# Performance work log

Measured on AMD Instinct MI355X. Metric: run time of the kernel, lower is better.

Reference implementation:

```python
import math
import jax, jax.numpy as jnp
import numpy as np

B, S, D, H, V = 8, 1024, 512, 8, 32000
HD = D // H


def _position_embedding(seq_len, d_model):
    pos = jnp.arange(seq_len, dtype=jnp.float32)[:, None]                 # [S,1]
    div = jnp.exp(jnp.arange(0, d_model, 2, dtype=jnp.float32) * (-math.log(10000.0) / d_model))  # [D/2]
    ang = pos * div                                                        # [S,D/2]
    # interleave sin (even cols) / cos (odd cols)
    return jnp.stack([jnp.sin(ang), jnp.cos(ang)], axis=-1).reshape(seq_len, d_model)


def _min_max_normalize(w):
    lo = jnp.min(w, axis=-1, keepdims=True)
    hi = jnp.max(w, axis=-1, keepdims=True)
    return (w - lo) / (hi - lo)


def _converable_mask(h, Wc, bc):
    bs, seq = h.shape[0], h.shape[1]
    half = seq // 2
    shift = math.ceil(seq / 2)
    width = jnp.einsum('bsd,od->bso', h, Wc)[..., 0] + bc[0]               # [B,S]
    width = _min_max_normalize(width)[..., None]                           # [B,S,1]
    origin = jnp.concatenate([jnp.linspace(1.0, 0.0, half),
                              jnp.linspace(0.0, 1.0, seq - half)])         # [S]
    origin_mask = 1.0 - jax.nn.sigmoid((origin[None, None, :] - width) * 100.0)  # [B,S,S]
    idx = (jnp.arange(seq - 1, -1, -1)[:, None] + jnp.arange(seq)[None, :]) % seq  # [S,S]
    idx = jnp.roll(idx, shift, axis=0)
    # torch.roll of a [1,S] row along dim 0 is a no-op
    cmp = idx >= jnp.arange(seq)[None, :]                                  # [S,S] bool
    move = jnp.concatenate([cmp[:shift], ~cmp[shift:]], axis=0)            # [S,S]
    gathered = jnp.take_along_axis(origin_mask, idx[None, :, :], axis=2)   # [B,S,S]
    return gathered * move.astype(origin_mask.dtype)


def setup_inputs():
    key = jax.random.key(0)
    ks = jax.random.split(key, 9)
    s_emb = 1.0
    s_hd = 1.0 / math.sqrt(HD)
    s_d = 1.0 / math.sqrt(D)
    return {
        'x':   jax.random.randint(ks[0], (B, S), 0, V),
        'emb': jax.random.normal(ks[1], (V, D), dtype=jnp.float32) * s_emb,
        'Wq':  jax.random.normal(ks[2], (HD, HD), dtype=jnp.float32) * s_hd,
        'Wk':  jax.random.normal(ks[3], (HD, HD), dtype=jnp.float32) * s_hd,
        'Wv':  jax.random.normal(ks[4], (HD, HD), dtype=jnp.float32) * s_hd,
        'Wo':  jax.random.normal(ks[5], (D, D), dtype=jnp.float32) * s_d,
        'bo':  jnp.zeros((D,), dtype=jnp.float32),
        'Wc':  jax.random.normal(ks[6], (1, D), dtype=jnp.float32) * s_d,
        'bc':  jnp.zeros((1,), dtype=jnp.float32),
    }


def reference(x, emb, Wq, Wk, Wv, Wo, bo, Wc, bc):
    h = emb[x] + _position_embedding(S, D)[None]                           # [B,S,D]
    mask = _converable_mask(h, Wc, bc)                                     # [B,S,S]
    hh = h.reshape(B, S, H, HD)
    q = jnp.einsum('bshd,od->bsho', hh, Wq)
    k = jnp.einsum('bshd,od->bsho', hh, Wk)
    v = jnp.einsum('bshd,od->bsho', hh, Wv)
    energy = jnp.einsum('bqhd,bkhd->bhqk', q, k)                           # [B,H,S,S]
    # mask [B,S,S] broadcasts as [1,B,S,S]; valid because B == H (as in original)
    energy = energy * mask
    attn = jax.nn.softmax(energy / math.sqrt(D), axis=3)
    out = jnp.einsum('bhqk,bkhd->bqhd', attn, v).reshape(B, S, D)
    out = out @ Wo.T + bo
    return (out, mask)
```

## Files before the change

kernel.cpp:

```cpp
#include <hip/hip_runtime.h>
#include <hip/hip_bf16.h>
#include <math.h>

#define Bn 8
#define Sn 1024
#define Dn 512
#define Hn 8
#define HDn 64

typedef __bf16 bf16x8 __attribute__((ext_vector_type(8)));
typedef __bf16 bf16x4 __attribute__((ext_vector_type(4)));
typedef __bf16 bf16x2 __attribute__((ext_vector_type(2)));
typedef float  f32x4  __attribute__((ext_vector_type(4)));
typedef float  f32x16 __attribute__((ext_vector_type(16)));
typedef unsigned int u32x4 __attribute__((ext_vector_type(4)));
typedef int i32x2 __attribute__((ext_vector_type(2)));

__device__ __forceinline__ unsigned enc_f(float v) {
    unsigned u = __float_as_uint(v);
    return (u & 0x80000000u) ? ~u : (u | 0x80000000u);
}
__device__ __forceinline__ float dec_f(unsigned k) {
    unsigned u = (k & 0x80000000u) ? (k ^ 0x80000000u) : ~k;
    return __uint_as_float(u);
}

__global__ __launch_bounds__(256) void k_fused(
        const int* __restrict__ x, const float* __restrict__ emb,
        const float* __restrict__ Wc, const float* __restrict__ bc,
        const float* __restrict__ Wq, const float* __restrict__ Wk,
        const float* __restrict__ Wv,
        float* __restrict__ width, unsigned* __restrict__ lohi,
        __bf16* __restrict__ q, __bf16* __restrict__ k, __bf16* __restrict__ vt) {
    __shared__ __align__(16) __bf16 Xs[64][72];
    __shared__ __align__(16) __bf16 WqS[64][72];
    __shared__ __align__(16) __bf16 WkS[64][72];
    __shared__ __align__(16) __bf16 WvS[64][72];
    __shared__ float wtok[8];
    int t = threadIdx.x;
    int bs0 = blockIdx.x * 8;
    int m0 = blockIdx.x * 64;
    int w = t >> 6, lane = t & 63, quad = lane >> 4, li = lane & 15;

    {
        int token = t >> 5, l32 = t & 31;
        int bs = bs0 + token;
        int s = bs & (Sn - 1);
        int tok = x[bs];
        float wpart = 0.f;
        int row = token * 8 + ((l32 * 16) >> 6);
        #pragma unroll
        for (int j = 0; j < 4; ++j) {
            int d0 = l32 * 16 + j * 4;
            float4 ev = *(const float4*)&emb[(size_t)tok * Dn + d0];
            float4 wc = *(const float4*)&Wc[d0];
            float hv[4];
            #pragma unroll
            for (int i = 0; i < 4; ++i) {
                int d = d0 + i;
                float f = __expf((float)(d & ~1) * (-9.210340371976184f / 512.0f));
                float ang = (float)s * f;
                float pe = (d & 1) ? __cosf(ang) : __sinf(ang);
                hv[i] = (&ev.x)[i] + pe;
                wpart += hv[i] * (&wc.x)[i];
            }
            *(bf16x4*)&Xs[row][d0 & 63] =
                (bf16x4){(__bf16)hv[0], (__bf16)hv[1], (__bf16)hv[2], (__bf16)hv[3]};
        }
        #pragma unroll
        for (int off = 1; off < 32; off <<= 1) wpart += __shfl_xor(wpart, off);
        if (l32 == 0) { float wv = wpart + bc[0]; width[bs] = wv; wtok[token] = wv; }
    }
    #pragma unroll
    for (int it = 0; it < 4; ++it) {
        int e = (it * 256 + t) * 4; int r = e >> 6, c = e & 63;
        float4 qv = *(const float4*)&Wq[e];
        *(bf16x4*)&WqS[r][c] = (bf16x4){(__bf16)qv.x, (__bf16)qv.y, (__bf16)qv.z, (__bf16)qv.w};
        float4 kv = *(const float4*)&Wk[e];
        *(bf16x4*)&WkS[r][c] = (bf16x4){(__bf16)kv.x, (__bf16)kv.y, (__bf16)kv.z, (__bf16)kv.w};
        float4 vv = *(const float4*)&Wv[e];
        *(bf16x4*)&WvS[r][c] = (bf16x4){(__bf16)vv.x, (__bf16)vv.y, (__bf16)vv.z, (__bf16)vv.w};
    }
    __syncthreads();

    if (t == 0) {
        float mn = wtok[0], mx = wtok[0];
        #pragma unroll
        for (int i = 1; i < 8; ++i) { mn = fminf(mn, wtok[i]); mx = fmaxf(mx, wtok[i]); }
        int b = bs0 >> 10;
        atomicMin(&lohi[b], enc_f(mn));
        atomicMin(&lohi[8 + b], ~enc_f(mx));
    }

    bf16x8 A0 = *(const bf16x8*)&Xs[w * 16 + li][quad * 8];
    bf16x8 A1 = *(const bf16x8*)&Xs[w * 16 + li][32 + quad * 8];
    f32x4 aq[4], ak[4], av[4];
    #pragma unroll
    for (int n = 0; n < 4; ++n) {
        aq[n] = (f32x4){0.f,0.f,0.f,0.f}; ak[n] = aq[n]; av[n] = aq[n];
        bf16x8 Bq0 = *(const bf16x8*)&WqS[n * 16 + li][quad * 8];
        bf16x8 Bq1 = *(const bf16x8*)&WqS[n * 16 + li][32 + quad * 8];
        aq[n] = __builtin_amdgcn_mfma_f32_16x16x32_bf16(A0, Bq0, aq[n], 0, 0, 0);
        aq[n] = __builtin_amdgcn_mfma_f32_16x16x32_bf16(A1, Bq1, aq[n], 0, 0, 0);
        bf16x8 Bk0 = *(const bf16x8*)&WkS[n * 16 + li][quad * 8];
        bf16x8 Bk1 = *(const bf16x8*)&WkS[n * 16 + li][32 + quad * 8];
        ak[n] = __builtin_amdgcn_mfma_f32_16x16x32_bf16(A0, Bk0, ak[n], 0, 0, 0);
        ak[n] = __builtin_amdgcn_mfma_f32_16x16x32_bf16(A1, Bk1, ak[n], 0, 0, 0);
        bf16x8 Bv0 = *(const bf16x8*)&WvS[n * 16 + li][quad * 8];
        bf16x8 Bv1 = *(const bf16x8*)&WvS[n * 16 + li][32 + quad * 8];
        av[n] = __builtin_amdgcn_mfma_f32_16x16x32_bf16(A0, Bv0, av[n], 0, 0, 0);
        av[n] = __builtin_amdgcn_mfma_f32_16x16x32_bf16(A1, Bv1, av[n], 0, 0, 0);
    }

    const float SCALE = 0.04419417382415922f;
    __syncthreads();
    #pragma unroll
    for (int n = 0; n < 4; ++n)
        #pragma unroll
        for (int r = 0; r < 4; ++r) {
            int row = w * 16 + quad * 4 + r, col = n * 16 + li;
            WkS[row][col] = (__bf16)(aq[n][r] * SCALE);
            WvS[row][col] = (__bf16)ak[n][r];
            WqS[row][col] = (__bf16)av[n][r];
        }
    __syncthreads();

    {
        int row = t >> 2, part = (t & 3) * 16;
        int Rg = m0 + row;
        int bsI = Rg >> 3, head = Rg & 7;
        int bq = bsI >> 10, sq = bsI & (Sn - 1);
        size_t base = (((size_t)(bq * Hn + head)) * Sn + sq) * HDn + part;
        *(bf16x8*)&q[base]     = *(bf16x8*)&WkS[row][part];
        *(bf16x8*)&q[base + 8] = *(bf16x8*)&WkS[row][part + 8];
        *(bf16x8*)&k[base]     = *(bf16x8*)&WvS[row][part];
        *(bf16x8*)&k[base + 8] = *(bf16x8*)&WvS[row][part + 8];
    }

    __bf16 (*Vs)[72] = WqS;
    int bs0i = m0 >> 3;
    int b = bs0i >> 10, s0l = bs0i & (Sn - 1);
    #pragma unroll
    for (int i = 0; i < 2; ++i) {
        int p = t + 256 * i;
        int head = p >> 6, o = p & 63;
        __bf16 tmp[8];
        #pragma unroll
        for (int j = 0; j < 8; ++j) tmp[j] = Vs[j * 8 + head][o];
        *(bf16x8*)&vt[(((size_t)(b * Hn + head)) * HDn + o) * Sn + s0l] = *(bf16x8*)tmp;
    }
}

__global__ void k_mask(const float* __restrict__ width, const unsigned* __restrict__ lohi,
                       float* __restrict__ mask_out) {
    int bs = blockIdx.x;
    int b = bs >> 10;
    int s = bs & (Sn - 1);
    float lo = dec_f(lohi[b]);
    float hi = dec_f(~lohi[8 + b]);
    float wn = (width[bs] - lo) / (hi - lo);
    for (int t = threadIdx.x; t < Sn; t += 256) {
        int it = (t - s + 1535) & (Sn - 1);
        float origin = (it < 512) ? (1.0f - (float)it * (1.0f / 511.0f))
                                  : ((float)(it - 512) * (1.0f / 511.0f));
        float z = (origin - wn) * 100.0f;
        float om;
        if (z >= 0.0f) { float e = __expf(-z); om = e / (1.0f + e); }
        else           { float e = __expf(z);  om = 1.0f / (1.0f + e); }
        bool cmpv = (it >= t);
        bool mv = (s < 512) ? cmpv : !cmpv;
        mask_out[(size_t)bs * Sn + t] = mv ? om : 0.0f;
    }
}

__global__ __launch_bounds__(256, 2) void k_attn(
        const __bf16* __restrict__ q, const __bf16* __restrict__ k,
        const __bf16* __restrict__ vt, const float* __restrict__ mask,
        __bf16* __restrict__ ao) {
    __shared__ __align__(16) __bf16 Ks[2][64][72];
    __shared__ __align__(16) __bf16 Vt[2][64][72];
    int blk = blockIdx.x;
    int hh = blk & 7;
    int qt = (blk >> 3) & 7;
    int b  = blk >> 6;
    int bh = b * Hn + hh;
    int q0 = qt * 128;
    int t = threadIdx.x;
    int w = t >> 6, lane = t & 63, hi5 = lane >> 5, l31 = lane & 31;

    const __bf16* qbase  = q  + ((size_t)bh * Sn + q0 + w * 32) * HDn;
    const __bf16* kbase  = k  + (size_t)bh * Sn * HDn;
    const __bf16* vtbase = vt + (size_t)bh * HDn * Sn;
    const float* mq = mask + ((size_t)hh * Sn + q0 + w * 32 + l31) * Sn;

    bf16x8 Qf[4];
    #pragma unroll
    for (int c = 0; c < 4; ++c)
        Qf[c] = *(const bf16x8*)&qbase[(size_t)l31 * HDn + c * 16 + hi5 * 8];

    int sr0 = t >> 3, sc0 = (t & 7) * 8;
    bf16x8 pk0, pk1, pv0, pv1;
    pk0 = *(const bf16x8*)&kbase[(size_t)sr0 * HDn + sc0];
    pk1 = *(const bf16x8*)&kbase[(size_t)(sr0 + 32) * HDn + sc0];
    pv0 = *(const bf16x8*)&vtbase[(size_t)sr0 * Sn + sc0];
    pv1 = *(const bf16x8*)&vtbase[(size_t)(sr0 + 32) * Sn + sc0];
    *(bf16x8*)&Ks[0][sr0][sc0] = pk0;
    *(bf16x8*)&Ks[0][sr0 + 32][sc0] = pk1;
    *(bf16x8*)&Vt[0][sr0][sc0] = pv0;
    *(bf16x8*)&Vt[0][sr0 + 32][sc0] = pv1;
    __syncthreads();

    f32x16 OT[2];
    OT[0] = (f32x16){0.f,0.f,0.f,0.f,0.f,0.f,0.f,0.f,0.f,0.f,0.f,0.f,0.f,0.f,0.f,0.f};
    OT[1] = OT[0];
    float rs = 0.f;

    for (int ti = 0; ti < 16; ++ti) {
        int cur = ti & 1;

        float4 mk[2][4];
        #pragma unroll
        for (int kg = 0; kg < 2; ++kg)
            #pragma unroll
            for (int g = 0; g < 4; ++g)
                mk[kg][g] = *(const float4*)&mq[ti * 64 + kg * 32 + g * 8 + hi5 * 4];

        if (ti < 15) {
            int k0n = (ti + 1) * 64;
            pk0 = *(const bf16x8*)&kbase[(size_t)(k0n + sr0) * HDn + sc0];
            pk1 = *(const bf16x8*)&kbase[(size_t)(k0n + sr0 + 32) * HDn + sc0];
            pv0 = *(const bf16x8*)&vtbase[(size_t)sr0 * Sn + k0n + sc0];
            pv1 = *(const bf16x8*)&vtbase[(size_t)(sr0 + 32) * Sn + k0n + sc0];
        }

        bf16x8 Kf[2][4], Vf[2][4];
        #pragma unroll
        for (int h = 0; h < 2; ++h)
            #pragma unroll
            for (int c = 0; c < 4; ++c)
                Kf[h][c] = *(const bf16x8*)&Ks[cur][h * 32 + l31][c * 16 + hi5 * 8];
        #pragma unroll
        for (int h = 0; h < 2; ++h)
            #pragma unroll
            for (int c = 0; c < 4; ++c)
                Vf[h][c] = *(const bf16x8*)&Vt[cur][h * 32 + l31][c * 16 + hi5 * 8];

        f32x16 St[2];
        St[0] = (f32x16){0.f,0.f,0.f,0.f,0.f,0.f,0.f,0.f,0.f,0.f,0.f,0.f,0.f,0.f,0.f,0.f};
        St[1] = St[0];
        __builtin_amdgcn_s_setprio(1);
        #pragma unroll
        for (int c = 0; c < 4; ++c) {
            St[0] = __builtin_amdgcn_mfma_f32_32x32x16_bf16(Kf[0][c], Qf[c], St[0], 0, 0, 0);
            St[1] = __builtin_amdgcn_mfma_f32_32x32x16_bf16(Kf[1][c], Qf[c], St[1], 0, 0, 0);
        }
        __builtin_amdgcn_s_setprio(0);

        unsigned pkd[2][4][2];
        #pragma unroll
        for (int kg = 0; kg < 2; ++kg) {
            #pragma unroll
            for (int g = 0; g < 4; ++g) {
                float p0 = __expf(St[kg][4 * g + 0] * mk[kg][g].x);
                float p1 = __expf(St[kg][4 * g + 1] * mk[kg][g].y);
                float p2 = __expf(St[kg][4 * g + 2] * mk[kg][g].z);
                float p3 = __expf(St[kg][4 * g + 3] * mk[kg][g].w);
                rs += (p0 + p1) + (p2 + p3);
                bf16x2 plo = { (__bf16)p0, (__bf16)p1 };
                bf16x2 phi = { (__bf16)p2, (__bf16)p3 };
                pkd[kg][g][0] = __builtin_bit_cast(unsigned, plo);
                pkd[kg][g][1] = __builtin_bit_cast(unsigned, phi);
            }
        }

        __builtin_amdgcn_s_setprio(1);
        #pragma unroll
        for (int c = 0; c < 4; ++c) {
            const int kg = c >> 1, gA = 2 * (c & 1), gB = gA + 1;
            i32x2 r0 = __builtin_amdgcn_permlane32_swap(
                (int)pkd[kg][gA][0], (int)pkd[kg][gB][0], false, false);
            i32x2 r1 = __builtin_amdgcn_permlane32_swap(
                (int)pkd[kg][gA][1], (int)pkd[kg][gB][1], false, false);
            u32x4 du;
            du[0] = (unsigned)r0[0];
            du[1] = (unsigned)r1[0];
            du[2] = (unsigned)r0[1];
            du[3] = (unsigned)r1[1];
            bf16x8 Pf = __builtin_bit_cast(bf16x8, du);
            OT[0] = __builtin_amdgcn_mfma_f32_32x32x16_bf16(Vf[0][c], Pf, OT[0], 0, 0, 0);
            OT[1] = __builtin_amdgcn_mfma_f32_32x32x16_bf16(Vf[1][c], Pf, OT[1], 0, 0, 0);
        }
        __builtin_amdgcn_s_setprio(0);

        if (ti < 15) {
            *(bf16x8*)&Ks[cur ^ 1][sr0][sc0] = pk0;
            *(bf16x8*)&Ks[cur ^ 1][sr0 + 32][sc0] = pk1;
            *(bf16x8*)&Vt[cur ^ 1][sr0][sc0] = pv0;
            *(bf16x8*)&Vt[cur ^ 1][sr0 + 32][sc0] = pv1;
            __syncthreads();
        }
    }

    rs += __shfl_xor(rs, 32);
    float inv = __fdividef(1.0f, rs);

    size_t orow = ((size_t)b * Sn + q0 + w * 32 + l31) * Dn + hh * HDn;
    #pragma unroll
    for (int og = 0; og < 2; ++og)
        #pragma unroll
        for (int g2 = 0; g2 < 4; ++g2) {
            bf16x4 ov = { (__bf16)(OT[og][4 * g2 + 0] * inv),
                          (__bf16)(OT[og][4 * g2 + 1] * inv),
                          (__bf16)(OT[og][4 * g2 + 2] * inv),
                          (__bf16)(OT[og][4 * g2 + 3] * inv) };
            *(bf16x4*)&ao[orow + og * 32 + g2 * 8 + hi5 * 4] = ov;
        }
}

__global__ __launch_bounds__(256) void k_proj(
        const __bf16* __restrict__ ao, const float* __restrict__ Wo,
        const float* __restrict__ bo, float* __restrict__ out) {
    __shared__ __align__(16) __bf16 As[64][72];
    __shared__ __align__(16) __bf16 Bs[64][72];
    __shared__ __align__(16) float  Os[64][68];
    int bm = blockIdx.x >> 3;
    int bn = blockIdx.x & 7;
    int m0 = bm * 64, n0 = bn * 64;
    int t = threadIdx.x;
    int w = t >> 6, lane = t & 63, quad = lane >> 4, li = lane & 15;

    f32x4 O[4];
    #pragma unroll
    for (int n = 0; n < 4; ++n) O[n] = (f32x4){0.f, 0.f, 0.f, 0.f};

    for (int k0 = 0; k0 < Dn; k0 += 64) {
        if (k0) __syncthreads();
        #pragma unroll
        for (int it = 0; it < 2; ++it) {
            int e = (it * 256 + t) * 8; int r = e >> 6, c = e & 63;
            *(bf16x8*)&As[r][c] = *(const bf16x8*)&ao[(size_t)(m0 + r) * Dn + k0 + c];
        }
        #pragma unroll
        for (int it = 0; it < 4; ++it) {
            int e = (it * 256 + t) * 4; int r = e >> 6, c = e & 63;
            float4 wv = *(const float4*)&Wo[(size_t)(n0 + r) * Dn + k0 + c];
            *(bf16x4*)&Bs[r][c] = (bf16x4){(__bf16)wv.x, (__bf16)wv.y, (__bf16)wv.z, (__bf16)wv.w};
        }
        __syncthreads();

        bf16x8 A0 = *(const bf16x8*)&As[w * 16 + li][quad * 8];
        bf16x8 A1 = *(const bf16x8*)&As[w * 16 + li][32 + quad * 8];
        #pragma unroll
        for (int n = 0; n < 4; ++n) {
            bf16x8 B0 = *(const bf16x8*)&Bs[n * 16 + li][quad * 8];
            O[n] = __builtin_amdgcn_mfma_f32_16x16x32_bf16(A0, B0, O[n], 0, 0, 0);
            bf16x8 B1 = *(const bf16x8*)&Bs[n * 16 + li][32 + quad * 8];
            O[n] = __builtin_amdgcn_mfma_f32_16x16x32_bf16(A1, B1, O[n], 0, 0, 0);
        }
    }

    #pragma unroll
    for (int n = 0; n < 4; ++n) {
        float bias = bo[n0 + n * 16 + li];
        #pragma unroll
        for (int r = 0; r < 4; ++r)
            Os[w * 16 + quad * 4 + r][n * 16 + li] = O[n][r] + bias;
    }
    __syncthreads();
    {
        int row = t >> 2, part = (t & 3) * 16;
        size_t base = (size_t)(m0 + row) * Dn + n0 + part;
        #pragma unroll
        for (int j = 0; j < 4; ++j)
            *(float4*)&out[base + j * 4] = *(const float4*)&Os[row][part + j * 4];
    }
}

extern "C" void kernel_launch(void* const* d_in, const int* in_sizes, int n_in,
                              void* d_out, int out_size, void* d_ws, size_t ws_size,
                              hipStream_t stream) {
    const int*   x   = (const int*)d_in[0];
    const float* emb = (const float*)d_in[1];
    const float* Wq  = (const float*)d_in[2];
    const float* Wk  = (const float*)d_in[3];
    const float* Wv  = (const float*)d_in[4];
    const float* Wo  = (const float*)d_in[5];
    const float* bo  = (const float*)d_in[6];
    const float* Wc  = (const float*)d_in[7];
    const float* bc  = (const float*)d_in[8];

    float* ws      = (float*)d_ws;
    float* width   = ws;
    unsigned* lohi = (unsigned*)(width + Bn * Sn);
    __bf16* qb   = (__bf16*)(ws + Bn * Sn + 16);
    __bf16* kb   = qb + (size_t)Bn * Sn * Dn;
    __bf16* vtb  = kb + (size_t)Bn * Sn * Dn;
    __bf16* ao   = vtb + (size_t)Bn * Sn * Dn;

    float* out      = (float*)d_out;
    float* mask_out = out + (size_t)Bn * Sn * Dn;

    hipMemsetAsync(lohi, 0xFF, 16 * sizeof(unsigned), stream);
    k_fused<<<(Bn * Sn) / 8, 256, 0, stream>>>(x, emb, Wc, bc, Wq, Wk, Wv,
                                               width, lohi, qb, kb, vtb);
    k_mask<<<Bn * Sn, 256, 0, stream>>>(width, lohi, mask_out);
    k_attn<<<Bn * Hn * (Sn / 128), 256, 0, stream>>>(qb, kb, vtb, mask_out, ao);
    k_proj<<<(Bn * Sn / 64) * (Dn / 64), 256, 0, stream>>>(ao, Wo, bo, out);
}
```

Baseline: 216.7 us.

## Fuse mask generation into attention kernel and recompute mask instead of loading

```diff
diff --git a/kernel.cpp b/kernel.cpp
--- a/kernel.cpp
+++ b/kernel.cpp
@@ -16,27 +16,17 @@
 typedef unsigned int u32x4 __attribute__((ext_vector_type(4)));
 typedef int i32x2 __attribute__((ext_vector_type(2)));
 
-__device__ __forceinline__ unsigned enc_f(float v) {
-    unsigned u = __float_as_uint(v);
-    return (u & 0x80000000u) ? ~u : (u | 0x80000000u);
-}
-__device__ __forceinline__ float dec_f(unsigned k) {
-    unsigned u = (k & 0x80000000u) ? (k ^ 0x80000000u) : ~k;
-    return __uint_as_float(u);
-}
-
 __global__ __launch_bounds__(256) void k_fused(
         const int* __restrict__ x, const float* __restrict__ emb,
         const float* __restrict__ Wc, const float* __restrict__ bc,
         const float* __restrict__ Wq, const float* __restrict__ Wk,
         const float* __restrict__ Wv,
-        float* __restrict__ width, unsigned* __restrict__ lohi,
+        float* __restrict__ width,
         __bf16* __restrict__ q, __bf16* __restrict__ k, __bf16* __restrict__ vt) {
     __shared__ __align__(16) __bf16 Xs[64][72];
     __shared__ __align__(16) __bf16 WqS[64][72];
     __shared__ __align__(16) __bf16 WkS[64][72];
     __shared__ __align__(16) __bf16 WvS[64][72];
-    __shared__ float wtok[8];
     int t = threadIdx.x;
     int bs0 = blockIdx.x * 8;
     int m0 = blockIdx.x * 64;
@@ -69,7 +59,7 @@
         }
         #pragma unroll
         for (int off = 1; off < 32; off <<= 1) wpart += __shfl_xor(wpart, off);
-        if (l32 == 0) { float wv = wpart + bc[0]; width[bs] = wv; wtok[token] = wv; }
+        if (l32 == 0) width[bs] = wpart + bc[0];
     }
     #pragma unroll
     for (int it = 0; it < 4; ++it) {
@@ -82,15 +72,6 @@
         *(bf16x4*)&WvS[r][c] = (bf16x4){(__bf16)vv.x, (__bf16)vv.y, (__bf16)vv.z, (__bf16)vv.w};
     }
     __syncthreads();
-
-    if (t == 0) {
-        float mn = wtok[0], mx = wtok[0];
-        #pragma unroll
-        for (int i = 1; i < 8; ++i) { mn = fminf(mn, wtok[i]); mx = fmaxf(mx, wtok[i]); }
-        int b = bs0 >> 10;
-        atomicMin(&lohi[b], enc_f(mn));
-        atomicMin(&lohi[8 + b], ~enc_f(mx));
-    }
 
     bf16x8 A0 = *(const bf16x8*)&Xs[w * 16 + li][quad * 8];
     bf16x8 A1 = *(const bf16x8*)&Xs[w * 16 + li][32 + quad * 8];
@@ -151,34 +132,22 @@
     }
 }
 
-__global__ void k_mask(const float* __restrict__ width, const unsigned* __restrict__ lohi,
-                       float* __restrict__ mask_out) {
-    int bs = blockIdx.x;
-    int b = bs >> 10;
-    int s = bs & (Sn - 1);
-    float lo = dec_f(lohi[b]);
-    float hi = dec_f(~lohi[8 + b]);
-    float wn = (width[bs] - lo) / (hi - lo);
-    for (int t = threadIdx.x; t < Sn; t += 256) {
-        int it = (t - s + 1535) & (Sn - 1);
-        float origin = (it < 512) ? (1.0f - (float)it * (1.0f / 511.0f))
-                                  : ((float)(it - 512) * (1.0f / 511.0f));
-        float z = (origin - wn) * 100.0f;
-        float om;
-        if (z >= 0.0f) { float e = __expf(-z); om = e / (1.0f + e); }
-        else           { float e = __expf(z);  om = 1.0f / (1.0f + e); }
-        bool cmpv = (it >= t);
-        bool mv = (s < 512) ? cmpv : !cmpv;
-        mask_out[(size_t)bs * Sn + t] = mv ? om : 0.0f;
-    }
+__device__ __forceinline__ float mask_val(int it, int kcol, float wn, bool flip) {
+    float origin = (fabsf((float)it - 511.5f) - 0.5f) * (1.0f / 511.0f);
+    float z = (origin - wn) * 100.0f;
+    float e = __expf(-fabsf(z));
+    float om = __fdividef((z >= 0.0f) ? e : 1.0f, 1.0f + e);
+    bool mv = (it >= kcol) ^ flip;
+    return mv ? om : 0.0f;
 }
 
 __global__ __launch_bounds__(256, 2) void k_attn(
         const __bf16* __restrict__ q, const __bf16* __restrict__ k,
-        const __bf16* __restrict__ vt, const float* __restrict__ mask,
-        __bf16* __restrict__ ao) {
+        const __bf16* __restrict__ vt, const float* __restrict__ width,
+        float* __restrict__ mask_out, __bf16* __restrict__ ao) {
     __shared__ __align__(16) __bf16 Ks[2][64][72];
     __shared__ __align__(16) __bf16 Vt[2][64][72];
+    __shared__ float red[16];
     int blk = blockIdx.x;
     int hh = blk & 7;
     int qt = (blk >> 3) & 7;
@@ -191,12 +160,25 @@
     const __bf16* qbase  = q  + ((size_t)bh * Sn + q0 + w * 32) * HDn;
     const __bf16* kbase  = k  + (size_t)bh * Sn * HDn;
     const __bf16* vtbase = vt + (size_t)bh * HDn * Sn;
-    const float* mq = mask + ((size_t)hh * Sn + q0 + w * 32 + l31) * Sn;
+    const float*  wrow   = width + (size_t)hh * Sn;
 
     bf16x8 Qf[4];
     #pragma unroll
     for (int c = 0; c < 4; ++c)
         Qf[c] = *(const bf16x8*)&qbase[(size_t)l31 * HDn + c * 16 + hi5 * 8];
+
+    float mnv, mxv;
+    {
+        float4 w4 = *(const float4*)&wrow[t * 4];
+        mnv = fminf(fminf(w4.x, w4.y), fminf(w4.z, w4.w));
+        mxv = fmaxf(fmaxf(w4.x, w4.y), fmaxf(w4.z, w4.w));
+        #pragma unroll
+        for (int off = 1; off < 64; off <<= 1) {
+            mnv = fminf(mnv, __shfl_xor(mnv, off));
+            mxv = fmaxf(mxv, __shfl_xor(mxv, off));
+        }
+        if (lane == 0) { red[w] = mnv; red[8 + w] = mxv; }
+    }
 
     int sr0 = t >> 3, sc0 = (t & 7) * 8;
     bf16x8 pk0, pk1, pv0, pv1;
@@ -210,6 +192,15 @@
     *(bf16x8*)&Vt[0][sr0 + 32][sc0] = pv1;
     __syncthreads();
 
+    mnv = fminf(fminf(red[0], red[1]), fminf(red[2], red[3]));
+    mxv = fmaxf(fmaxf(red[8], red[9]), fmaxf(red[10], red[11]));
+    float rinv = __fdividef(1.0f, mxv - mnv);
+
+    int srow = q0 + w * 32 + l31;
+    float wn = (wrow[srow] - mnv) * rinv;
+    int c0 = 1535 - srow;
+    bool flip = srow >= 512;
+
     f32x16 OT[2];
     OT[0] = (f32x16){0.f,0.f,0.f,0.f,0.f,0.f,0.f,0.f,0.f,0.f,0.f,0.f,0.f,0.f,0.f,0.f};
     OT[1] = OT[0];
@@ -217,13 +208,6 @@
 
     for (int ti = 0; ti < 16; ++ti) {
         int cur = ti & 1;
-
-        float4 mk[2][4];
-        #pragma unroll
-        for (int kg = 0; kg < 2; ++kg)
-            #pragma unroll
-            for (int g = 0; g < 4; ++g)
-                mk[kg][g] = *(const float4*)&mq[ti * 64 + kg * 32 + g * 8 + hi5 * 4];
 
         if (ti < 15) {
             int k0n = (ti + 1) * 64;
@@ -233,26 +217,16 @@
             pv1 = *(const bf16x8*)&vtbase[(size_t)(sr0 + 32) * Sn + k0n + sc0];
         }
 
-        bf16x8 Kf[2][4], Vf[2][4];
-        #pragma unroll
-        for (int h = 0; h < 2; ++h)
-            #pragma unroll
-            for (int c = 0; c < 4; ++c)
-                Kf[h][c] = *(const bf16x8*)&Ks[cur][h * 32 + l31][c * 16 + hi5 * 8];
-        #pragma unroll
-        for (int h = 0; h < 2; ++h)
-            #pragma unroll
-            for (int c = 0; c < 4; ++c)
-                Vf[h][c] = *(const bf16x8*)&Vt[cur][h * 32 + l31][c * 16 + hi5 * 8];
-
         f32x16 St[2];
         St[0] = (f32x16){0.f,0.f,0.f,0.f,0.f,0.f,0.f,0.f,0.f,0.f,0.f,0.f,0.f,0.f,0.f,0.f};
         St[1] = St[0];
         __builtin_amdgcn_s_setprio(1);
         #pragma unroll
         for (int c = 0; c < 4; ++c) {
-            St[0] = __builtin_amdgcn_mfma_f32_32x32x16_bf16(Kf[0][c], Qf[c], St[0], 0, 0, 0);
-            St[1] = __builtin_amdgcn_mfma_f32_32x32x16_bf16(Kf[1][c], Qf[c], St[1], 0, 0, 0);
+            bf16x8 K0 = *(const bf16x8*)&Ks[cur][l31][c * 16 + hi5 * 8];
+            St[0] = __builtin_amdgcn_mfma_f32_32x32x16_bf16(K0, Qf[c], St[0], 0, 0, 0);
+            bf16x8 K1 = *(const bf16x8*)&Ks[cur][32 + l31][c * 16 + hi5 * 8];
+            St[1] = __builtin_amdgcn_mfma_f32_32x32x16_bf16(K1, Qf[c], St[1], 0, 0, 0);
         }
         __builtin_amdgcn_s_setprio(0);
 
@@ -261,13 +235,17 @@
         for (int kg = 0; kg < 2; ++kg) {
             #pragma unroll
             for (int g = 0; g < 4; ++g) {
-                float p0 = __expf(St[kg][4 * g + 0] * mk[kg][g].x);
-                float p1 = __expf(St[kg][4 * g + 1] * mk[kg][g].y);
-                float p2 = __expf(St[kg][4 * g + 2] * mk[kg][g].z);
-                float p3 = __expf(St[kg][4 * g + 3] * mk[kg][g].w);
-                rs += (p0 + p1) + (p2 + p3);
-                bf16x2 plo = { (__bf16)p0, (__bf16)p1 };
-                bf16x2 phi = { (__bf16)p2, (__bf16)p3 };
+                float pv[4];
+                #pragma unroll
+                for (int j = 0; j < 4; ++j) {
+                    int kabs = ti * 64 + kg * 32 + g * 8 + hi5 * 4 + j;
+                    int itx = (kabs + c0) & 1023;
+                    float val = mask_val(itx, kabs, wn, flip);
+                    pv[j] = __expf(St[kg][4 * g + j] * val);
+                    rs += pv[j];
+                }
+                bf16x2 plo = { (__bf16)pv[0], (__bf16)pv[1] };
+                bf16x2 phi = { (__bf16)pv[2], (__bf16)pv[3] };
                 pkd[kg][g][0] = __builtin_bit_cast(unsigned, plo);
                 pkd[kg][g][1] = __builtin_bit_cast(unsigned, phi);
             }
@@ -287,8 +265,10 @@
             du[2] = (unsigned)r0[1];
             du[3] = (unsigned)r1[1];
             bf16x8 Pf = __builtin_bit_cast(bf16x8, du);
-            OT[0] = __builtin_amdgcn_mfma_f32_32x32x16_bf16(Vf[0][c], Pf, OT[0], 0, 0, 0);
-            OT[1] = __builtin_amdgcn_mfma_f32_32x32x16_bf16(Vf[1][c], Pf, OT[1], 0, 0, 0);
+            bf16x8 V0 = *(const bf16x8*)&Vt[cur][l31][c * 16 + hi5 * 8];
+            OT[0] = __builtin_amdgcn_mfma_f32_32x32x16_bf16(V0, Pf, OT[0], 0, 0, 0);
+            bf16x8 V1 = *(const bf16x8*)&Vt[cur][32 + l31][c * 16 + hi5 * 8];
+            OT[1] = __builtin_amdgcn_mfma_f32_32x32x16_bf16(V1, Pf, OT[1], 0, 0, 0);
         }
         __builtin_amdgcn_s_setprio(0);
 
@@ -315,6 +295,26 @@
                           (__bf16)(OT[og][4 * g2 + 3] * inv) };
             *(bf16x4*)&ao[orow + og * 32 + g2 * 8 + hi5 * 4] = ov;
         }
+
+    {
+        float* mbase = mask_out + (size_t)hh * Sn * Sn;
+        int col = t * 4;
+        #pragma unroll
+        for (int r = 0; r < 16; ++r) {
+            int row = q0 + b * 16 + r;
+            float wnr = (wrow[row] - mnv) * rinv;
+            bool fl = row >= 512;
+            int c0r = 1535 - row;
+            float4 ov;
+            #pragma unroll
+            for (int j = 0; j < 4; ++j) {
+                int cc = col + j;
+                int itx = (cc + c0r) & 1023;
+                (&ov.x)[j] = mask_val(itx, cc, wnr, fl);
+            }
+            *(float4*)&mbase[(size_t)row * Sn + col] = ov;
+        }
+    }
 }
 
 __global__ __launch_bounds__(256) void k_proj(
@@ -391,8 +391,7 @@
 
     float* ws      = (float*)d_ws;
     float* width   = ws;
-    unsigned* lohi = (unsigned*)(width + Bn * Sn);
-    __bf16* qb   = (__bf16*)(ws + Bn * Sn + 16);
+    __bf16* qb   = (__bf16*)(ws + Bn * Sn);
     __bf16* kb   = qb + (size_t)Bn * Sn * Dn;
     __bf16* vtb  = kb + (size_t)Bn * Sn * Dn;
     __bf16* ao   = vtb + (size_t)Bn * Sn * Dn;
@@ -400,10 +399,9 @@
     float* out      = (float*)d_out;
     float* mask_out = out + (size_t)Bn * Sn * Dn;
 
-    hipMemsetAsync(lohi, 0xFF, 16 * sizeof(unsigned), stream);
     k_fused<<<(Bn * Sn) / 8, 256, 0, stream>>>(x, emb, Wc, bc, Wq, Wk, Wv,
-                                               width, lohi, qb, kb, vtb);
-    k_mask<<<Bn * Sn, 256, 0, stream>>>(width, lohi, mask_out);
-    k_attn<<<Bn * Hn * (Sn / 128), 256, 0, stream>>>(qb, kb, vtb, mask_out, ao);
+                                               width, qb, kb, vtb);
+    k_attn<<<Bn * Hn * (Sn / 128), 256, 0, stream>>>(qb, kb, vtb, width,
+                                                     mask_out, ao);
     k_proj<<<(Bn * Sn / 64) * (Dn / 64), 256, 0, stream>>>(ao, Wo, bo, out);
 }
```

Result: no change. 220.2 us (+1.6%).
